# Optimization experiments

Measured on AMD Instinct MI355X. Metric: run time of the kernel, lower is better.

## Reference

```python
import jax, jax.numpy as jnp
import numpy as np

# dims
B, T, D, H, DFF, NTYPE = 8, 1024, 512, 8, 1024, 341
HD = D // H                    # 64 head dim
NUM_AXES = 1
DPR = D // H // (NUM_AXES + 1) # 32 dims rotated per axis
EPS = 1e-5
THETA = 10000.0


def layernorm(x, g, b):
    m = jnp.mean(x, axis=-1, keepdims=True)
    v = jnp.mean((x - m) ** 2, axis=-1, keepdims=True)
    return (x - m) * jax.lax.rsqrt(v + EPS) * g + b


def swiglu(x):
    a, gate = jnp.split(x, 2, axis=-1)
    return jax.nn.silu(gate) * a


def apply_rope(x, pos):
    # x: [B,H,T,DPR], pos: [B,T] float positions (possibly non-integer / scrambled order)
    inv_freq = 1.0 / (THETA ** (jnp.arange(0, DPR, 2, dtype=jnp.float32) / DPR))  # [DPR/2]
    freqs = pos[:, None, :, None] * inv_freq          # [B,1,T,DPR/2]
    cos = jnp.repeat(jnp.cos(freqs), 2, axis=-1)      # each freq repeated twice -> [B,1,T,DPR]
    sin = jnp.repeat(jnp.sin(freqs), 2, axis=-1)
    x1 = x[..., 0::2]
    x2 = x[..., 1::2]
    rot = jnp.stack([-x2, x1], axis=-1).reshape(x.shape)  # rotate_half, interleaved pairs
    return x * cos + rot * sin


def setup_inputs() -> dict:
    key = jax.random.key(0)
    ks = jax.random.split(key, 16)
    s = lambda d: 1.0 / np.sqrt(d)
    return {
        "x_type": jax.random.randint(ks[0], (B, T + 1), 0, NTYPE),
        "x_value": jax.random.normal(ks[1], (B, T, D), dtype=jnp.float32),
        "seq_order": jax.random.uniform(ks[2], (B, T + 1), dtype=jnp.float32) * T,
        "W_attn": jax.random.normal(ks[3], (D, 3 * D), dtype=jnp.float32) * s(D),
        "type_emb": jax.random.normal(ks[4], (NTYPE, 2 * D), dtype=jnp.float32) * 0.02,
        "ln1_g": jnp.ones((D,), jnp.float32),
        "ln1_b": jnp.zeros((D,), jnp.float32),
        "ln2_g": jnp.ones((D,), jnp.float32),
        "ln2_b": jnp.zeros((D,), jnp.float32),
        "W1": jax.random.normal(ks[5], (D, 2 * DFF), dtype=jnp.float32) * s(D),
        "b1": jnp.zeros((2 * DFF,), jnp.float32),
        "W2": jax.random.normal(ks[6], (DFF, D), dtype=jnp.float32) * s(DFF),
        "b2": jnp.zeros((D,), jnp.float32),
    }


def reference(x_type, x_value, seq_order, W_attn, type_emb, ln1_g, ln1_b, ln2_g, ln2_b, W1, b1, W2, b2):
    # --- attention sublayer ---
    h = layernorm(x_value, ln1_g, ln1_b)                  # [B,T,D]
    qkv = h @ W_attn                                      # [B,T,3D]
    q, k, v = jnp.split(qkv, 3, axis=-1)
    emb = type_emb[x_type]                                # [B,T+1,2D]
    q_embed, k_embed = jnp.split(emb, 2, axis=-1)
    q = q + q_embed[:, :-1]
    k = k + k_embed[:, 1:]
    # [B,H,T,HD]
    to_heads = lambda t: t.reshape(B, T, H, HD).transpose(0, 2, 1, 3)
    q, k, v = to_heads(q), to_heads(k), to_heads(v)
    # rotate first DPR dims with (shifted) seq_order; remaining dims untouched
    q = jnp.concatenate([apply_rope(q[..., :DPR], seq_order[:, :-1]), q[..., DPR:]], axis=-1)
    k = jnp.concatenate([apply_rope(k[..., :DPR], seq_order[:, 1:]), k[..., DPR:]], axis=-1)
    # causal SDPA
    scores = jnp.einsum("bhqd,bhkd->bhqk", q, k) / jnp.sqrt(jnp.float32(HD))
    causal = jnp.tril(jnp.ones((T, T), dtype=bool))
    scores = jnp.where(causal, scores, -jnp.inf)
    attn = jax.nn.softmax(scores, axis=-1)
    out = jnp.einsum("bhqk,bhkd->bhqd", attn, v)          # [B,H,T,HD]
    out = out.transpose(0, 2, 1, 3).reshape(B, T, D)
    x = x_value + out
    # --- SwiGLU FFN sublayer ---
    h2 = layernorm(x, ln2_g, ln2_b)
    ff = swiglu(h2 @ W1 + b1) @ W2 + b2
    return x + ff
```

## Files before the change

### kernel.cpp

```cpp
#include <hip/hip_runtime.h>
#include <stdint.h>
#include <math.h>

typedef unsigned short u16;
typedef unsigned int u32;
typedef __attribute__((ext_vector_type(8))) short bf16x8;
typedef __attribute__((ext_vector_type(4))) float f32x4;
typedef __attribute__((ext_vector_type(2))) float f32x2;
typedef __attribute__((ext_vector_type(2))) u16 u16x2;
typedef __attribute__((ext_vector_type(8))) u16 u16x8;
typedef __attribute__((ext_vector_type(2))) u32 u32x2;

#define B_ 8
#define T_ 1024
#define D_ 512
#define H_ 8
#define TP1 1025
#define QSCALE 0.1803368801111204f

__device__ __forceinline__ u16 f2b(float f) {
  union { float f; u32 u; } v; v.f = f;
  return (u16)((v.u + 0x7fffu + ((v.u >> 16) & 1u)) >> 16);
}
__device__ __forceinline__ void gld16(const void* g, void* l) {
  __builtin_amdgcn_global_load_lds((const __attribute__((address_space(1))) u32*)g,
                                   (__attribute__((address_space(3))) u32*)l, 16, 0, 0);
}
__device__ __forceinline__ f32x4 mfma16(bf16x8 a, bf16x8 b, f32x4 c) {
  return __builtin_amdgcn_mfma_f32_16x16x32_bf16(a, b, c, 0, 0, 0);
}
__device__ __forceinline__ u32 cvtpk(float lo, float hi) {
  u32 r;
  asm("v_cvt_pk_bf16_f32 %0, %1, %2" : "=v"(r) : "v"(lo), "v"(hi));
  return r;
}
union U8 { u32 u[4]; bf16x8 v; };

#define WAITV(N) asm volatile("s_waitcnt vmcnt(" #N ")" ::: "memory")

__global__ __launch_bounds__(256) void prep_kernel(const float* __restrict__ W_attn,
    const float* __restrict__ W1, const float* __restrict__ W2,
    const float* __restrict__ seq,
    u16* __restrict__ WtA, u16* __restrict__ W1i, u16* __restrict__ W2t,
    float* __restrict__ cq, float* __restrict__ sq_,
    float* __restrict__ ck, float* __restrict__ sk,
    const float* __restrict__ xv, const float* __restrict__ ln1g,
    const float* __restrict__ ln1b, u16* __restrict__ hbuf) {
  int bid = blockIdx.x, tid = threadIdx.x;
  if (bid >= 1088) {
    int row = (bid - 1088) * 4 + (tid >> 6);
    int lane = tid & 63;
    const float* xr = xv + (size_t)row * D_ + lane * 8;
    f32x4 v0 = *(const f32x4*)xr;
    f32x4 v1 = *(const f32x4*)(xr + 4);
    float s = 0.f, sq = 0.f;
    #pragma unroll
    for (int j = 0; j < 4; j++) { s += v0[j] + v1[j]; sq += v0[j] * v0[j] + v1[j] * v1[j]; }
    #pragma unroll
    for (int m = 1; m < 64; m <<= 1) { s += __shfl_xor(s, m); sq += __shfl_xor(sq, m); }
    float mean = s * (1.f / D_);
    float var = sq * (1.f / D_) - mean * mean;
    float rstd = rsqrtf(var + 1e-5f);
    f32x4 g0 = *(const f32x4*)(ln1g + lane * 8);
    f32x4 g1 = *(const f32x4*)(ln1g + lane * 8 + 4);
    f32x4 b0 = *(const f32x4*)(ln1b + lane * 8);
    f32x4 b1 = *(const f32x4*)(ln1b + lane * 8 + 4);
    u16x8 o;
    #pragma unroll
    for (int j = 0; j < 4; j++) {
      o[j]     = f2b((v0[j] - mean) * rstd * g0[j] + b0[j]);
      o[4 + j] = f2b((v1[j] - mean) * rstd * g1[j] + b1[j]);
    }
    *(u16x8*)(hbuf + (size_t)row * D_ + lane * 8) = o;
    return;
  }
  if (bid >= 576) {
    int i = (bid - 576) * 256 + tid;
    int p = i & 15, bt = i >> 4, b = bt >> 10, t = bt & 1023;
    float inv = expf(-(float)p * 0.5756462732485115f);
    float aq = seq[b * TP1 + t] * inv;
    float ak = seq[b * TP1 + t + 1] * inv;
    cq[i] = cosf(aq); sq_[i] = sinf(aq);
    ck[i] = cosf(ak); sk[i] = sinf(ak);
    return;
  }
  __shared__ u16 lt[64][65];
  const float* src; u16* dst; int ld, Kd, k0, r0; bool ilv = false;
  if (bid < 192) {
    src = W_attn; dst = WtA; ld = 1536; Kd = 512;
    k0 = (bid & 7) * 64; r0 = (bid >> 3) * 64;
  } else if (bid < 448) {
    int t = bid - 192;
    src = W1; dst = W1i; ld = 2048; Kd = 512; ilv = true;
    k0 = (t & 7) * 64; r0 = (t >> 3) * 64;
  } else {
    int t = bid - 448;
    src = W2; dst = W2t; ld = 512; Kd = 1024;
    k0 = (t & 15) * 64; r0 = (t >> 4) * 64;
  }
  int nl = tid & 63;
  int scol, rloc;
  if (ilv) {
    if (nl < 32) { scol = (r0 >> 1) + nl;          rloc = ((nl >> 4) << 5) + (nl & 15); }
    else         { scol = 1024 + (r0 >> 1) + (nl - 32); rloc = (((nl - 32) >> 4) << 5) + 16 + (nl & 15); }
  } else { scol = r0 + nl; rloc = nl; }
  #pragma unroll
  for (int it = 0; it < 16; it++) {
    int kl = (tid >> 6) * 16 + it;
    lt[rloc][kl] = f2b(src[(size_t)(k0 + kl) * ld + scol]);
  }
  __syncthreads();
  #pragma unroll
  for (int it = 0; it < 16; it++) {
    int rl = (tid >> 6) * 16 + it;
    dst[(size_t)(r0 + rl) * Kd + k0 + nl] = lt[rl][nl];
  }
}

__global__ __launch_bounds__(256) void ln_kernel(const float* __restrict__ x,
    const float* __restrict__ g, const float* __restrict__ bta, u16* __restrict__ out) {
  int row = blockIdx.x * 4 + (threadIdx.x >> 6);
  int lane = threadIdx.x & 63;
  const float* xr = x + (size_t)row * D_ + lane * 8;
  f32x4 v0 = *(const f32x4*)xr;
  f32x4 v1 = *(const f32x4*)(xr + 4);
  float s = 0.f, sq = 0.f;
  #pragma unroll
  for (int j = 0; j < 4; j++) { s += v0[j] + v1[j]; sq += v0[j] * v0[j] + v1[j] * v1[j]; }
  #pragma unroll
  for (int m = 1; m < 64; m <<= 1) { s += __shfl_xor(s, m); sq += __shfl_xor(sq, m); }
  float mean = s * (1.f / D_);
  float var = sq * (1.f / D_) - mean * mean;
  float rstd = rsqrtf(var + 1e-5f);
  f32x4 g0 = *(const f32x4*)(g + lane * 8);
  f32x4 g1 = *(const f32x4*)(g + lane * 8 + 4);
  f32x4 b0 = *(const f32x4*)(bta + lane * 8);
  f32x4 b1 = *(const f32x4*)(bta + lane * 8 + 4);
  u16x8 o;
  #pragma unroll
  for (int j = 0; j < 4; j++) {
    o[j]     = f2b((v0[j] - mean) * rstd * g0[j] + b0[j]);
    o[4 + j] = f2b((v1[j] - mean) * rstd * g1[j] + b1[j]);
  }
  *(u16x8*)(out + (size_t)row * D_ + lane * 8) = o;
}

__global__ __launch_bounds__(256) void gemm_qkv(const u16* __restrict__ A,
    const u16* __restrict__ Bt,
    const int* __restrict__ x_type, const float* __restrict__ type_emb,
    const float* __restrict__ rqc, const float* __restrict__ rqs,
    const float* __restrict__ rkc, const float* __restrict__ rks,
    u16* __restrict__ qT, u16* __restrict__ kT, u16* __restrict__ vT) {
  __shared__ u16 lsmem[6 * 4096];
  u16* lA = lsmem;
  u16* lB = lsmem + 3 * 4096;
  const int K = 512, NK = 16;
  const int tid = threadIdx.x, lane = tid & 63, w = tid >> 6;
  const int wm = w >> 1, wn = w & 1;
  int swz = (blockIdx.x & 7) * 96 + (blockIdx.x >> 3);
  int byy = swz / 12, bxx = swz - byy * 12;
  const size_t bm = (size_t)byy * 128;
  const size_t bn = (size_t)bxx * 128;

  const int r0 = tid >> 2;
  const int cs = ((tid & 3) ^ ((r0 >> 1) & 3)) * 8;
  const u16* a0 = A + (bm + r0) * K + cs;
  const u16* a1 = A + (bm + 64 + r0) * K + cs;
  const u16* b0 = Bt + (bn + r0) * K + cs;
  const u16* b1p = Bt + (bn + 64 + r0) * K + cs;

  int aoff[4], boff[4];
  #pragma unroll
  for (int i = 0; i < 4; i++) {
    int ra = wm * 64 + i * 16 + (lane & 15);
    aoff[i] = ra * 64 + (((lane >> 4) ^ ((ra >> 1) & 3)) * 16);
    int rb = wn * 64 + i * 16 + (lane & 15);
    boff[i] = rb * 64 + (((lane >> 4) ^ ((rb >> 1) & 3)) * 16);
  }

  auto stage = [&](int j, int buf) {
    char* ad = (char*)lA + buf * 8192 + w * 1024;
    char* bd = (char*)lB + buf * 8192 + w * 1024;
    gld16(a0 + j * 32, ad);
    gld16(a1 + j * 32, ad + 4096);
    gld16(b0 + j * 32, bd);
    gld16(b1p + j * 32, bd + 4096);
  };
  f32x4 acc[4][4] = {};
  auto compute = [&](int buf) {
    const char* lAc = (const char*)lA + buf * 8192;
    const char* lBc = (const char*)lB + buf * 8192;
    bf16x8 af[4], bf[4];
    #pragma unroll
    for (int i = 0; i < 4; i++) af[i] = *(const bf16x8*)(lAc + aoff[i]);
    #pragma unroll
    for (int n = 0; n < 4; n++) bf[n] = *(const bf16x8*)(lBc + boff[n]);
    __builtin_amdgcn_s_setprio(1);
    #pragma unroll
    for (int i = 0; i < 4; i++)
      #pragma unroll
      for (int n = 0; n < 4; n++)
        acc[i][n] = mfma16(af[i], bf[n], acc[i][n]);
    __builtin_amdgcn_s_setprio(0);
  };

  stage(0, 0);
  stage(1, 1);
  int cur = 0;
  for (int j = 0; j < NK - 1; j++) {
    WAITV(4);
    __builtin_amdgcn_s_barrier();
    if (j + 2 < NK) { int nb = cur + 2; if (nb >= 3) nb -= 3; stage(j + 2, nb); }
    compute(cur);
    cur = (cur + 1 == 3) ? 0 : cur + 1;
  }
  WAITV(0);
  __builtin_amdgcn_s_barrier();
  compute(cur);

  const int region = (int)(bn >> 9);
  __syncthreads();
  u16 (*tbuf)[136] = (u16(*)[136])lsmem;
  const int bb = (int)(bm >> 10);
  const int t0 = (int)(bm & 1023);

  if (region < 2) {
    #pragma unroll
    for (int i = 0; i < 4; i++) {
      #pragma unroll
      for (int jj = 0; jj < 4; jj++) {
        int rl = wm * 64 + i * 16 + (lane >> 4) * 4 + jj;
        int row = (int)bm + rl;
        int b = row >> 10, t = row & 1023;
        int ty = x_type[b * TP1 + t + region];
        const float* rc = (region == 0) ? rqc : rkc;
        const float* rs = (region == 0) ? rqs : rks;
        #pragma unroll
        for (int n = 0; n < 4; n++) {
          int cl = wn * 64 + n * 16 + (lane & 15);
          int cloc = ((int)bn - region * 512) + cl;
          int hd = cloc & 63;
          float v = acc[i][n][jj] + type_emb[(size_t)ty * 1024 + region * 512 + cloc];
          float vp = __shfl_xor(v, 1);
          if (hd < 32) {
            int p = hd >> 1;
            float c = rc[row * 16 + p], s = rs[row * 16 + p];
            v = (hd & 1) ? (v * c + vp * s) : (v * c - vp * s);
          }
          if (region == 0) v *= QSCALE;
          tbuf[rl][cl] = f2b(v);
        }
      }
    }
    __syncthreads();
    u16* dst = (region == 0) ? qT : kT;
    const int h0 = (((int)bn - region * 512) >> 6);
    #pragma unroll
    for (int p = 0; p < 8; p++) {
      int chunk = p * 256 + tid;
      int tl = chunk >> 4;
      int cc = (chunk & 15) * 8;
      u16x8 o = *(const u16x8*)&tbuf[tl][cc];
      *(u16x8*)(dst + ((size_t)(bb * 8 + h0 + (cc >> 6)) * T_ + t0 + tl) * 64 +
                (cc & 63)) = o;
    }
  } else {
    #pragma unroll
    for (int i = 0; i < 4; i++) {
      #pragma unroll
      for (int n = 0; n < 4; n++) {
        int cl = wn * 64 + n * 16 + (lane & 15);
        #pragma unroll
        for (int jj = 0; jj < 4; jj++) {
          int r = wm * 64 + i * 16 + (lane >> 4) * 4 + jj;
          tbuf[cl][r] = f2b(acc[i][n][jj]);
        }
      }
    }
    __syncthreads();
    const int h0 = ((int)bn - 1024) >> 6;
    const size_t rbase = (size_t)(bb * 8 + h0) * 64;
    #pragma unroll
    for (int p = 0; p < 8; p++) {
      int rl = p * 16 + (tid >> 4);
      int c8 = (tid & 15) * 8;
      u16x8 o = *(const u16x8*)&tbuf[rl][c8];
      *(u16x8*)(vT + (rbase + rl) * T_ + t0 + c8) = o;
    }
  }
}

__global__ __launch_bounds__(512) void gemm_ff1(const u16* __restrict__ A,
    const u16* __restrict__ Bt, const float* __restrict__ b1,
    u16* __restrict__ outp) {
  __shared__ u16 lsmem[24576];
  u16* lA = lsmem;
  u16* lB = lsmem + 16384;
  const int K = 512;
  const int tid = threadIdx.x, lane = tid & 63, w = tid >> 6;
  const int wm = w >> 2, wn = w & 3;
  int swz = (blockIdx.x & 7) * 64 + (blockIdx.x >> 3);
  int byy = swz >> 4, bxx = swz & 15;
  const size_t bm = (size_t)byy * 256;
  const size_t bn = (size_t)bxx * 128;

  const int r0 = tid >> 2;
  const int cs = ((tid & 3) ^ ((r0 >> 1) & 3)) * 8;
  const u16* a0 = A + (bm + r0) * K + cs;
  const u16* a1 = A + (bm + 128 + r0) * K + cs;
  const u16* b0 = Bt + (bn + r0) * K + cs;

  int aoff[8], boff[2];
  #pragma unroll
  for (int i = 0; i < 8; i++) {
    int ra = wm * 128 + i * 16 + (lane & 15);
    aoff[i] = ra * 64 + (((lane >> 4) ^ ((ra >> 1) & 3)) * 16);
  }
  #pragma unroll
  for (int n = 0; n < 2; n++) {
    int rb = wn * 32 + n * 16 + (lane & 15);
    boff[n] = rb * 64 + (((lane >> 4) ^ ((rb >> 1) & 3)) * 16);
  }

  auto stage = [&](int k0, int buf) {
    char* ad = (char*)lA + buf * 16384 + w * 1024;
    char* bd = (char*)lB + buf * 8192 + w * 1024;
    gld16(a0 + k0, ad);
    gld16(a1 + k0, ad + 8192);
    gld16(b0 + k0, bd);
  };

  f32x4 acc[8][2] = {};
  stage(0, 0);
  __syncthreads();
  int cur = 0;
  for (int k0 = 0; k0 < K; k0 += 32) {
    if (k0 + 32 < K) stage(k0 + 32, cur ^ 1);
    const char* lAc = (const char*)lA + cur * 16384;
    const char* lBc = (const char*)lB + cur * 8192;
    bf16x8 bf[2];
    #pragma unroll
    for (int n = 0; n < 2; n++) bf[n] = *(const bf16x8*)(lBc + boff[n]);
    __builtin_amdgcn_s_setprio(1);
    #pragma unroll
    for (int i = 0; i < 8; i++) {
      bf16x8 af = *(const bf16x8*)(lAc + aoff[i]);
      acc[i][0] = mfma16(af, bf[0], acc[i][0]);
      acc[i][1] = mfma16(af, bf[1], acc[i][1]);
    }
    __builtin_amdgcn_s_setprio(0);
    __syncthreads();
    cur ^= 1;
  }
  __syncthreads();
  u16 (*tbuf)[72] = (u16(*)[72])lsmem;
  {
    int cl = wn * 16 + (lane & 15);
    int c = ((int)bn >> 1) + cl;
    float bav = b1[c], bgv = b1[1024 + c];
    #pragma unroll
    for (int i = 0; i < 8; i++) {
      #pragma unroll
      for (int jj = 0; jj < 4; jj++) {
        int rl = wm * 128 + i * 16 + (lane >> 4) * 4 + jj;
        float av = acc[i][0][jj] + bav;
        float gv = acc[i][1][jj] + bgv;
        float sg = gv / (1.f + expf(-gv));
        tbuf[rl][cl] = f2b(sg * av);
      }
    }
  }
  __syncthreads();
  {
    const int c0 = ((int)bn >> 1);
    #pragma unroll
    for (int p = 0; p < 4; p++) {
      int ch = p * 512 + tid;
      int rl = ch >> 3;
      int cc = (ch & 7) * 8;
      u16x8 o = *(const u16x8*)&tbuf[rl][cc];
      *(u16x8*)(outp + (size_t)((int)bm + rl) * 1024 + c0 + cc) = o;
    }
  }
}

__global__ __launch_bounds__(512) void gemm_ff2(const u16* __restrict__ A,
    const u16* __restrict__ Bt, const float* __restrict__ bias,
    float* __restrict__ C) {
  __shared__ u16 lA[3][4096];
  __shared__ u16 lB[3][4096];
  const int K = 1024, N = 512, NK = 32;
  const int tid = threadIdx.x, lane = tid & 63, w = tid >> 6;
  const int wm = w >> 2, wn = w & 3;
  int swz = (blockIdx.x & 7) * 32 + (blockIdx.x >> 3);
  int byy = swz >> 2, bxx = swz & 3;
  const size_t bm = (size_t)byy * 128;
  const size_t bn = (size_t)bxx * 128;

  const int r0 = tid >> 2;
  const int cs = ((tid & 3) ^ ((r0 >> 1) & 3)) * 8;
  const u16* a0 = A + (bm + r0) * K + cs;
  const u16* b0 = Bt + (bn + r0) * K + cs;

  int aoff[4], boff[2];
  #pragma unroll
  for (int i = 0; i < 4; i++) {
    int ra = wm * 64 + i * 16 + (lane & 15);
    aoff[i] = ra * 64 + (((lane >> 4) ^ ((ra >> 1) & 3)) * 16);
  }
  #pragma unroll
  for (int n = 0; n < 2; n++) {
    int rb = wn * 32 + n * 16 + (lane & 15);
    boff[n] = rb * 64 + (((lane >> 4) ^ ((rb >> 1) & 3)) * 16);
  }

  auto stage = [&](int j, int buf) {
    gld16(a0 + j * 32, (char*)lA + buf * 8192 + w * 1024);
    gld16(b0 + j * 32, (char*)lB + buf * 8192 + w * 1024);
  };
  f32x4 acc[4][2] = {};
  auto compute = [&](int buf) {
    const char* lAc = (const char*)lA + buf * 8192;
    const char* lBc = (const char*)lB + buf * 8192;
    bf16x8 af[4], bf[2];
    #pragma unroll
    for (int i = 0; i < 4; i++) af[i] = *(const bf16x8*)(lAc + aoff[i]);
    #pragma unroll
    for (int n = 0; n < 2; n++) bf[n] = *(const bf16x8*)(lBc + boff[n]);
    __builtin_amdgcn_s_setprio(1);
    #pragma unroll
    for (int i = 0; i < 4; i++)
      #pragma unroll
      for (int n = 0; n < 2; n++)
        acc[i][n] = mfma16(af[i], bf[n], acc[i][n]);
    __builtin_amdgcn_s_setprio(0);
  };

  stage(0, 0);
  stage(1, 1);
  int cur = 0;
  for (int j = 0; j < NK - 1; j++) {
    WAITV(2);
    __builtin_amdgcn_s_barrier();
    if (j + 2 < NK) { int nb = cur + 2; if (nb >= 3) nb -= 3; stage(j + 2, nb); }
    compute(cur);
    cur = (cur + 1 == 3) ? 0 : cur + 1;
  }
  WAITV(0);
  __builtin_amdgcn_s_barrier();
  compute(cur);

  #pragma unroll
  for (int i = 0; i < 4; i++) {
    size_t mrow = bm + wm * 64 + i * 16 + (lane >> 4) * 4;
    #pragma unroll
    for (int n = 0; n < 2; n++) {
      size_t col = bn + wn * 32 + n * 16 + (lane & 15);
      float bv = bias[col];
      #pragma unroll
      for (int jj = 0; jj < 4; jj++) {
        size_t idx = (mrow + jj) * (size_t)N + col;
        C[idx] = acc[i][n][jj] + bv + C[idx];
      }
    }
  }
}

__global__ __launch_bounds__(512, 4) void attn_kernel(const u16* __restrict__ qT,
    const u16* __restrict__ kT, const u16* __restrict__ vT,
    const float* __restrict__ xv, float* __restrict__ X) {
  int s0 = (blockIdx.x & 7) * 64 + (blockIdx.x >> 3);
  const int bh = ((blockIdx.x & 7) << 3) + (s0 & 7);
  const int qp = 7 - ((s0 >> 3) & 7);
  const int b = bh >> 3, h = bh & 7;
  const int tid = threadIdx.x, lane = tid & 63, w = tid >> 6;
  const int q = lane & 15, g = lane >> 4;
  __shared__ u16 lK[2][8192];
  __shared__ u16 lV[2][8192];

  const int qrow0 = qp * 128 + w * 16;
  bf16x8 qf[2];
  {
    const u16* qp_ = qT + ((size_t)bh * T_ + qrow0 + q) * 64 + g * 8;
    qf[0] = *(const bf16x8*)qp_;
    qf[1] = *(const bf16x8*)(qp_ + 32);
  }
  f32x4 acc[4] = {};
  float mr = -1e30f, lr = 0.f;

  const int sr = tid >> 3;
  const int scs = ((tid & 7) ^ (sr & 7)) * 8;
  const u16* kb = kT + ((size_t)bh * T_ + sr) * 64 + scs;
  const u16* vb = vT + ((size_t)bh * 64 + sr) * T_ + scs;

  auto stage = [&](int j, int buf) {
    char* kd = (char*)lK + buf * 16384 + w * 1024;
    char* vd = (char*)lV + buf * 16384 + w * 1024;
    gld16(kb + (size_t)j * 8192, kd);
    gld16(kb + (size_t)j * 8192 + 4096, kd + 8192);
    gld16(vb + j * 128, vd);
    gld16(vb + j * 128 + 64, vd + 8192);
  };

  const int jmax = qp + 1;
  stage(0, 0);
  __syncthreads();
  int cur = 0;
  for (int j = 0; j < jmax; j++) {
    if (j + 1 < jmax) stage(j + 1, cur ^ 1);
    const char* lKc = (const char*)lK + cur * 16384;
    const char* lVc = (const char*)lV + cur * 16384;

    f32x4 s[8] = {};
    __builtin_amdgcn_s_setprio(1);
    #pragma unroll
    for (int ka = 0; ka < 2; ka++) {
      #pragma unroll
      for (int n = 0; n < 8; n++) {
        bf16x8 kf = *(const bf16x8*)(lKc + (n >> 2) * 8192 + ((n & 3) * 16 + q) * 128 +
                                     (((ka * 4 + g) ^ (q & 7)) * 16));
        s[n] = mfma16(kf, qf[ka], s[n]);
      }
    }
    __builtin_amdgcn_s_setprio(0);
    if (j == jmax - 1) {
      int qrow = w * 16 + q;
      #pragma unroll
      for (int n = 0; n < 8; n++)
        #pragma unroll
        for (int i = 0; i < 4; i++)
          if (n * 16 + g * 4 + i > qrow) s[n][i] = -1e30f;
    }
    float mt = -1e30f;
    #pragma unroll
    for (int n = 0; n < 8; n++)
      mt = fmaxf(mt, fmaxf(fmaxf(s[n][0], s[n][1]), fmaxf(s[n][2], s[n][3])));
    mt = fmaxf(mt, __shfl_xor(mt, 16));
    mt = fmaxf(mt, __shfl_xor(mt, 32));
    if (__any(mt > mr + 8.f)) {
      float mnew = fmaxf(mr, mt);
      float sc = exp2f(mr - mnew);
      mr = mnew;
      lr *= sc;
      #pragma unroll
      for (int t = 0; t < 4; t++) acc[t] *= sc;
    }
    float ps = 0.f;
    U8 pa[4];
    #pragma unroll
    for (int kt = 0; kt < 4; kt++) {
      float p0[4], p1[4];
      #pragma unroll
      for (int i = 0; i < 4; i++) {
        p0[i] = exp2f(s[2 * kt][i] - mr);
        p1[i] = exp2f(s[2 * kt + 1][i] - mr);
        ps += p0[i] + p1[i];
      }
      pa[kt].u[0] = cvtpk(p0[0], p0[1]);
      pa[kt].u[1] = cvtpk(p0[2], p0[3]);
      pa[kt].u[2] = cvtpk(p1[0], p1[1]);
      pa[kt].u[3] = cvtpk(p1[2], p1[3]);
    }
    ps += __shfl_xor(ps, 16);
    ps += __shfl_xor(ps, 32);
    lr += ps;
    __builtin_amdgcn_s_setprio(1);
    #pragma unroll
    for (int t = 0; t < 4; t++) {
      #pragma unroll
      for (int kt = 0; kt < 4; kt++) {
        const char* vrh = lVc + (kt >> 1) * 8192 + (t * 16 + q) * 128 + (g & 1) * 8;
        int ktl = kt & 1;
        u32x2 lo = *(const u32x2*)(vrh + (((ktl * 4 + (g >> 1)) ^ (q & 7)) * 16));
        u32x2 hi = *(const u32x2*)(vrh + (((ktl * 4 + 2 + (g >> 1)) ^ (q & 7)) * 16));
        U8 af;
        af.u[0] = lo[0]; af.u[1] = lo[1]; af.u[2] = hi[0]; af.u[3] = hi[1];
        acc[t] = mfma16(af.v, pa[kt].v, acc[t]);
      }
    }
    __builtin_amdgcn_s_setprio(0);
    __syncthreads();
    cur ^= 1;
  }
  {
    float inv = 1.f / lr;
    size_t base = ((size_t)b * T_ + qrow0 + q) * D_ + h * 64 + g * 4;
    #pragma unroll
    for (int t = 0; t < 4; t++) {
      f32x4 r = *(const f32x4*)(xv + base + t * 16);
      f32x4 o;
      #pragma unroll
      for (int i = 0; i < 4; i++) o[i] = r[i] + acc[t][i] * inv;
      *(f32x4*)(X + base + t * 16) = o;
    }
  }
}

extern "C" void kernel_launch(void* const* d_in, const int* in_sizes, int n_in,
                              void* d_out, int out_size, void* d_ws, size_t ws_size,
                              hipStream_t stream) {
  const int*   x_type   = (const int*)d_in[0];
  const float* x_value  = (const float*)d_in[1];
  const float* seq      = (const float*)d_in[2];
  const float* W_attn   = (const float*)d_in[3];
  const float* type_emb = (const float*)d_in[4];
  const float* ln1_g    = (const float*)d_in[5];
  const float* ln1_b    = (const float*)d_in[6];
  const float* ln2_g    = (const float*)d_in[7];
  const float* ln2_b    = (const float*)d_in[8];
  const float* W1       = (const float*)d_in[9];
  const float* b1       = (const float*)d_in[10];
  const float* W2       = (const float*)d_in[11];
  const float* b2       = (const float*)d_in[12];
  float* out = (float*)d_out;
  char* ws = (char*)d_ws;

  u16*   WtA  = (u16*)(ws + 0);
  u16*   W1i  = (u16*)(ws + 1572864);
  u16*   W2t  = (u16*)(ws + 3670016);
  float* rqc  = (float*)(ws + 4718592);
  float* rqs  = (float*)(ws + 5242880);
  float* rkc  = (float*)(ws + 5767168);
  float* rks  = (float*)(ws + 6291456);
  u16*   hbuf = (u16*)(ws + 6815744);
  u16*   qTb  = (u16*)(ws + 15204352);
  u16*   kTb  = (u16*)(ws + 23592960);
  u16*   vTb  = (u16*)(ws + 31981568);
  u16*   ff1a = (u16*)(ws + 15204352);

  prep_kernel<<<3136, 256, 0, stream>>>(W_attn, W1, W2, seq, WtA, W1i, W2t,
                                        rqc, rqs, rkc, rks,
                                        x_value, ln1_g, ln1_b, hbuf);
  gemm_qkv<<<768, 256, 0, stream>>>(hbuf, WtA, x_type, type_emb,
                                    rqc, rqs, rkc, rks, qTb, kTb, vTb);
  attn_kernel<<<512, 512, 0, stream>>>(qTb, kTb, vTb, x_value, out);
  ln_kernel<<<B_ * T_ / 4, 256, 0, stream>>>(out, ln2_g, ln2_b, hbuf);
  gemm_ff1<<<512, 512, 0, stream>>>(hbuf, W1i, b1, ff1a);
  gemm_ff2<<<256, 512, 0, stream>>>(ff1a, W2t, b2, out);
}
```

Baseline: 119.1 us.

## Switch FF2 GEMM to double-buffered 64-wide K stages with full syncs

Replaces the FF2 GEMM's three-deep pipeline of 32-wide K slices with two buffers of 64-wide K slices. The loop count and barrier count are halved, and each barrier now uses __syncthreads instead of explicit vmcnt waits. The cost is less prefetch depth, because only one stage is in flight. A full __syncthreads wait also drains outstanding loads every iteration, which may expose memory latency.

```diff
diff --git a/kernel.cpp b/kernel.cpp
--- a/kernel.cpp
+++ b/kernel.cpp
@@ -387,9 +387,9 @@
 __global__ __launch_bounds__(512) void gemm_ff2(const u16* __restrict__ A,
     const u16* __restrict__ Bt, const float* __restrict__ bias,
     float* __restrict__ C) {
-  __shared__ u16 lA[3][4096];
-  __shared__ u16 lB[3][4096];
-  const int K = 1024, N = 512, NK = 32;
+  __shared__ u16 lA[2][8192];
+  __shared__ u16 lB[2][8192];
+  const int K = 1024, N = 512, NJ = 16;
   const int tid = threadIdx.x, lane = tid & 63, w = tid >> 6;
   const int wm = w >> 2, wn = w & 3;
   int swz = (blockIdx.x & 7) * 32 + (blockIdx.x >> 3);
@@ -415,40 +415,43 @@
   }
 
   auto stage = [&](int j, int buf) {
-    gld16(a0 + j * 32, (char*)lA + buf * 8192 + w * 1024);
-    gld16(b0 + j * 32, (char*)lB + buf * 8192 + w * 1024);
+    #pragma unroll
+    for (int kh = 0; kh < 2; kh++) {
+      int ko = j * 64 + kh * 32;
+      gld16(a0 + ko, (char*)lA + buf * 16384 + kh * 8192 + w * 1024);
+      gld16(b0 + ko, (char*)lB + buf * 16384 + kh * 8192 + w * 1024);
+    }
   };
   f32x4 acc[4][2] = {};
   auto compute = [&](int buf) {
-    const char* lAc = (const char*)lA + buf * 8192;
-    const char* lBc = (const char*)lB + buf * 8192;
-    bf16x8 af[4], bf[2];
-    #pragma unroll
-    for (int i = 0; i < 4; i++) af[i] = *(const bf16x8*)(lAc + aoff[i]);
-    #pragma unroll
-    for (int n = 0; n < 2; n++) bf[n] = *(const bf16x8*)(lBc + boff[n]);
-    __builtin_amdgcn_s_setprio(1);
-    #pragma unroll
-    for (int i = 0; i < 4; i++)
-      #pragma unroll
-      for (int n = 0; n < 2; n++)
-        acc[i][n] = mfma16(af[i], bf[n], acc[i][n]);
-    __builtin_amdgcn_s_setprio(0);
+    #pragma unroll
+    for (int kh = 0; kh < 2; kh++) {
+      const char* lAc = (const char*)lA + buf * 16384 + kh * 8192;
+      const char* lBc = (const char*)lB + buf * 16384 + kh * 8192;
+      bf16x8 af[4], bf[2];
+      #pragma unroll
+      for (int i = 0; i < 4; i++) af[i] = *(const bf16x8*)(lAc + aoff[i]);
+      #pragma unroll
+      for (int n = 0; n < 2; n++) bf[n] = *(const bf16x8*)(lBc + boff[n]);
+      __builtin_amdgcn_s_setprio(1);
+      #pragma unroll
+      for (int i = 0; i < 4; i++)
+        #pragma unroll
+        for (int n = 0; n < 2; n++)
+          acc[i][n] = mfma16(af[i], bf[n], acc[i][n]);
+      __builtin_amdgcn_s_setprio(0);
+    }
   };
 
   stage(0, 0);
-  stage(1, 1);
+  __syncthreads();
   int cur = 0;
-  for (int j = 0; j < NK - 1; j++) {
-    WAITV(2);
-    __builtin_amdgcn_s_barrier();
-    if (j + 2 < NK) { int nb = cur + 2; if (nb >= 3) nb -= 3; stage(j + 2, nb); }
+  for (int j = 0; j < NJ; j++) {
+    if (j + 1 < NJ) stage(j + 1, cur ^ 1);
     compute(cur);
-    cur = (cur + 1 == 3) ? 0 : cur + 1;
-  }
-  WAITV(0);
-  __builtin_amdgcn_s_barrier();
-  compute(cur);
+    __syncthreads();
+    cur ^= 1;
+  }
 
   #pragma unroll
   for (int i = 0; i < 4; i++) {
```

Measured after the change: 116.1 us (median of 2 runs). 1.03x faster.
